# Kernel tuning notes

Hardware: AMD Instinct MI355X
Metric: run time of the kernel (lower is better)

Reference implementation:

```python
import jax, jax.numpy as jnp
import numpy as np

N, E, D = 50000, 800000, 128  # nodes, edges, in_dim=out_dim
LN_EPS = 1e-5


def setup_inputs() -> dict:
    key = jax.random.key(0)
    ks = jax.random.split(key, 8)
    x = jax.random.normal(ks[0], (N, D), dtype=jnp.float32)
    edge_index = jax.random.randint(ks[1], (2, E), 0, N, dtype=jnp.int64)
    edge_attr = jax.random.normal(ks[2], (E, D), dtype=jnp.float32)
    # message_net: Linear(2D -> D); update_net: Linear(2D -> D) + LayerNorm(D)
    s_msg = 1.0 / np.sqrt(2 * D)
    s_upd = 1.0 / np.sqrt(2 * D)
    W_msg = jax.random.uniform(ks[3], (2 * D, D), jnp.float32, -s_msg, s_msg)
    b_msg = jax.random.uniform(ks[4], (D,), jnp.float32, -s_msg, s_msg)
    W_upd = jax.random.uniform(ks[5], (2 * D, D), jnp.float32, -s_upd, s_upd)
    b_upd = jax.random.uniform(ks[6], (D,), jnp.float32, -s_upd, s_upd)
    gamma = jnp.ones((D,), jnp.float32)
    beta = jnp.zeros((D,), jnp.float32)
    return {"x": x, "edge_index": edge_index, "edge_attr": edge_attr,
            "W_msg": W_msg, "b_msg": b_msg, "W_upd": W_upd, "b_upd": b_upd,
            "gamma": gamma, "beta": beta}


def reference(x, edge_index, edge_attr, W_msg, b_msg, W_upd, b_upd, gamma, beta):
    src, dst = edge_index[0], edge_index[1]
    n = x.shape[0]
    # per-edge message: relu(Linear(concat[x_src, edge_attr]))  -> [E, D]
    msg_in = jnp.concatenate([x[src], edge_attr], axis=-1)
    msg = jax.nn.relu(msg_in @ W_msg + b_msg)
    # masked scatter-mean over destination nodes (zeros for isolated nodes)
    summed = jax.ops.segment_sum(msg, dst, num_segments=n)  # [N, D]
    counts = jax.ops.segment_sum(jnp.ones((msg.shape[0],), x.dtype), dst, num_segments=n)
    mean_msg = summed / jnp.maximum(counts, 1.0)[:, None]
    # update: Linear(concat[x, mean_msg]) + LayerNorm, residual (in_dim==out_dim), relu
    h = jnp.concatenate([x, mean_msg], axis=-1) @ W_upd + b_upd
    mu = jnp.mean(h, axis=-1, keepdims=True)
    var = jnp.mean(jnp.square(h - mu), axis=-1, keepdims=True)
    h = (h - mu) * jax.lax.rsqrt(var + LN_EPS) * gamma + beta
    return jax.nn.relu(h + x)
```

## Files before the change

kernel.cpp:

```cpp
#include <hip/hip_runtime.h>

#define LN_EPS 1e-5f

typedef __bf16 bf16x8 __attribute__((ext_vector_type(8)));
typedef unsigned short ushort8v __attribute__((ext_vector_type(8)));
typedef float f32x4 __attribute__((ext_vector_type(4)));

__device__ __forceinline__ float bf16_to_f(unsigned short u) {
    unsigned int x = ((unsigned int)u) << 16;
    return __builtin_bit_cast(float, x);
}
__device__ __forceinline__ unsigned short f_to_bf16(float f) {
    unsigned int u = __builtin_bit_cast(unsigned int, f);
    u += 0x7FFFu + ((u >> 16) & 1u);
    return (unsigned short)(u >> 16);
}
__device__ __forceinline__ int idx_at(const int* base, int i, int is64) {
    return is64 ? base[(long long)i << 1] : base[i];
}

template<int BF16>
__device__ __forceinline__ bf16x8 load_frag(const void* base, size_t off) {
    if (BF16) {
        return *(const bf16x8*)((const unsigned short*)base + off);
    } else {
        const float* p = (const float*)base + off;
        f32x4 a = *(const f32x4*)p;
        f32x4 b = *(const f32x4*)(p + 4);
        ushort8v u;
        u[0] = f_to_bf16(a[0]); u[1] = f_to_bf16(a[1]);
        u[2] = f_to_bf16(a[2]); u[3] = f_to_bf16(a[3]);
        u[4] = f_to_bf16(b[0]); u[5] = f_to_bf16(b[1]);
        u[6] = f_to_bf16(b[2]); u[7] = f_to_bf16(b[3]);
        return __builtin_bit_cast(bf16x8, u);
    }
}
template<int BF16>
__device__ __forceinline__ float load_sc(const void* base, size_t i) {
    return BF16 ? bf16_to_f(((const unsigned short*)base)[i]) : ((const float*)base)[i];
}
template<int BF16>
__device__ __forceinline__ void store_out(void* out, size_t i, float v) {
    if (BF16) ((unsigned short*)out)[i] = f_to_bf16(v);
    else      ((float*)out)[i] = v;
}

__global__ void detect_kernel(const unsigned short* __restrict__ xu,
                              const unsigned int* __restrict__ ei,
                              int N, int* __restrict__ flags)
{
    if (threadIdx.x != 0 || blockIdx.x != 0) return;
    int inrange = 0;
    for (int i = 0; i < 64; ++i) {
        unsigned short u = xu[2 * i];
        int e = (u >> 7) & 0xFF;
        if (e >= 0x60 && e <= 0x8A) inrange++;
    }
    int isbf16 = (inrange >= 48) ? 1 : 0;

    int is64 = 1;
    for (int i = 0; i < 64; ++i) {
        unsigned int lo = ei[2 * i], hi = ei[2 * i + 1];
        if (hi != 0u || lo >= (unsigned int)N) { is64 = 0; break; }
    }
    flags[0] = is64;
    flags[1] = isbf16;
}

__global__ __launch_bounds__(256) void zero_kernel(float* __restrict__ p, int n4)
{
    int i = blockIdx.x * 256 + threadIdx.x;
    if (i < n4) {
        f32x4 z = {0.f, 0.f, 0.f, 0.f};
        ((f32x4*)p)[i] = z;
    }
}

__global__ __launch_bounds__(256) void hist_kernel(
    const int* __restrict__ eidx, int* __restrict__ ecnt,
    const int* __restrict__ flags, int E)
{
    int e = blockIdx.x * 256 + threadIdx.x;
    if (e >= E) return;
    const int is64 = flags[0];
    const int* dstp = eidx + (is64 ? 2 * E : E);
    atomicAdd(&ecnt[idx_at(dstp, e, is64)], 1);
}

__global__ __launch_bounds__(1024) void scan_kernel(
    const int* __restrict__ ecnt, int* __restrict__ cursor, int N)
{
    __shared__ int sums[1024];
    const int t = threadIdx.x;
    const int chunk = (N + 1023) >> 10;
    const int s0 = t * chunk;
    const int s1 = (s0 + chunk < N) ? s0 + chunk : N;
    int sum = 0;
    for (int i = s0; i < s1; ++i) sum += ecnt[i];
    sums[t] = sum;
    __syncthreads();
    for (int ofs = 1; ofs < 1024; ofs <<= 1) {
        int v = sums[t];
        int add = (t >= ofs) ? sums[t - ofs] : 0;
        __syncthreads();
        sums[t] = v + add;
        __syncthreads();
    }
    int run = (t == 0) ? 0 : sums[t - 1];
    for (int i = s0; i < s1; ++i) { cursor[i] = run; run += ecnt[i]; }
}

__global__ __launch_bounds__(256) void scatter_kernel(
    const int* __restrict__ eidx, int* __restrict__ cursor,
    int* __restrict__ sorted_e, const int* __restrict__ flags, int E)
{
    int e = blockIdx.x * 256 + threadIdx.x;
    if (e >= E) return;
    const int is64 = flags[0];
    const int* dstp = eidx + (is64 ? 2 * E : E);
    int d = idx_at(dstp, e, is64);
    int pos = atomicAdd(&cursor[d], 1);
    sorted_e[pos] = e;
}

template<int BF16>
__global__ __launch_bounds__(256) void prep_transpose(
    const void* __restrict__ Wm, const void* __restrict__ Wu,
    unsigned short* __restrict__ WmT, unsigned short* __restrict__ WuT,
    const int* __restrict__ flags)
{
    if (flags[1] != BF16) return;
    int idx = blockIdx.x * 256 + threadIdx.x;
    int k = idx >> 7;
    int n = idx & 127;
    unsigned short wm, wu;
    if (BF16) {
        wm = ((const unsigned short*)Wm)[idx];
        wu = ((const unsigned short*)Wu)[idx];
    } else {
        wm = f_to_bf16(((const float*)Wm)[idx]);
        wu = f_to_bf16(((const float*)Wu)[idx]);
    }
    WmT[n * 256 + k] = wm;
    WuT[n * 256 + k] = wu;
}

template<int BF16>
__global__ __launch_bounds__(256) void edge_kernel(
    const void* __restrict__ x, const int* __restrict__ eidx,
    const void* __restrict__ ea, const unsigned short* __restrict__ WmT,
    const void* __restrict__ b_msg,
    float* __restrict__ sumbuf, const int* __restrict__ sorted_e,
    const int* __restrict__ flags, int E)
{
    if (flags[1] != BF16) return;
    const int is64 = flags[0];
    const int* srcp = eidx;
    const int* dstp = eidx + (is64 ? 2 * E : E);

    __shared__ int   eS[128];
    __shared__ int   dS[128];
    __shared__ float strip[2][16][132];

    const int pbase = blockIdx.x * 128;
    const int tid  = threadIdx.x;
    const int w    = tid >> 6;
    const int l    = tid & 63;
    const int m    = l & 15;
    const int quad = l >> 4;
    int valid = E - pbase; if (valid > 128) valid = 128;

    if (tid < 128) {
        int p = pbase + tid;
        int pc = p < E ? p : E - 1;
        int e = sorted_e[pc];
        eS[tid] = e;
        dS[tid] = idx_at(dstp, e, is64);
    }

    bf16x8 bfrag[2][8];
#pragma unroll
    for (int nt = 0; nt < 2; ++nt) {
        const unsigned short* p = WmT + (w * 32 + nt * 16 + m) * 256 + quad * 8;
#pragma unroll
        for (int kk = 0; kk < 8; ++kk)
            bfrag[nt][kk] = *(const bf16x8*)(p + kk * 32);
    }
    const float bias0 = load_sc<BF16>(b_msg, w * 32 + m);
    const float bias1 = load_sc<BF16>(b_msg, w * 32 + 16 + m);

    __syncthreads();

    int   cur_d   = -1;
    float cur_sum = 0.f;
    int   first   = 1;

    for (int mt = 0; mt < 8; ++mt) {
        const int b = mt & 1;
        const int e_a = eS[mt * 16 + m];
        const int sa  = idx_at(srcp, e_a, is64);
        const size_t xoff = (size_t)sa  * 128 + quad * 8;
        const size_t eoff = (size_t)e_a * 128 + quad * 8;

        f32x4 acc0 = {0.f, 0.f, 0.f, 0.f};
        f32x4 acc1 = {0.f, 0.f, 0.f, 0.f};
#pragma unroll
        for (int kk = 0; kk < 4; ++kk) {
            bf16x8 af = load_frag<BF16>(x, xoff + kk * 32);
            acc0 = __builtin_amdgcn_mfma_f32_16x16x32_bf16(af, bfrag[0][kk], acc0, 0, 0, 0);
            acc1 = __builtin_amdgcn_mfma_f32_16x16x32_bf16(af, bfrag[1][kk], acc1, 0, 0, 0);
        }
#pragma unroll
        for (int kk = 0; kk < 4; ++kk) {
            bf16x8 af = load_frag<BF16>(ea, eoff + kk * 32);
            acc0 = __builtin_amdgcn_mfma_f32_16x16x32_bf16(af, bfrag[0][kk + 4], acc0, 0, 0, 0);
            acc1 = __builtin_amdgcn_mfma_f32_16x16x32_bf16(af, bfrag[1][kk + 4], acc1, 0, 0, 0);
        }

#pragma unroll
        for (int i = 0; i < 4; ++i) {
            float v0 = acc0[i] + bias0; v0 = v0 > 0.f ? v0 : 0.f;
            float v1 = acc1[i] + bias1; v1 = v1 > 0.f ? v1 : 0.f;
            strip[b][quad * 4 + i][w * 32 + m]      = v0;
            strip[b][quad * 4 + i][w * 32 + 16 + m] = v1;
        }
        __syncthreads();

        if (tid < 128) {
            int rmax = valid - mt * 16; if (rmax > 16) rmax = 16;
            for (int r = 0; r < rmax; ++r) {
                int   d = dS[mt * 16 + r];
                float v = strip[b][r][tid];
                if (d == cur_d) {
                    cur_sum += v;
                } else {
                    if (cur_d >= 0) {
                        float* p = &sumbuf[(size_t)cur_d * 128 + tid];
                        if (first) { atomicAdd(p, cur_sum); first = 0; }
                        else       { *p = cur_sum; }
                    }
                    cur_d = d; cur_sum = v;
                }
            }
        }
    }
    if (tid < 128 && cur_d >= 0)
        atomicAdd(&sumbuf[(size_t)cur_d * 128 + tid], cur_sum);
}

template<int BF16>
__global__ __launch_bounds__(256) void node_kernel(
    const void* __restrict__ x,
    const float* __restrict__ sumbuf, const int* __restrict__ counts,
    const unsigned short* __restrict__ WuT, const void* __restrict__ b_upd,
    const void* __restrict__ gamma_, const void* __restrict__ beta_,
    void* __restrict__ out, const int* __restrict__ flags, int N)
{
    if (flags[1] != BF16) return;

    __shared__ float redS[4][64];
    __shared__ float redQ[4][64];
    __shared__ float muS[64];
    __shared__ float rsS[64];

    const int rbase = blockIdx.x * 64;
    const int tid  = threadIdx.x;
    const int w    = tid >> 6;
    const int l    = tid & 63;
    const int m    = l & 15;
    const int quad = l >> 4;

    bf16x8 bfrag[2][8];
#pragma unroll
    for (int nt = 0; nt < 2; ++nt) {
        const unsigned short* p = WuT + (w * 32 + nt * 16 + m) * 256 + quad * 8;
#pragma unroll
        for (int kk = 0; kk < 8; ++kk)
            bfrag[nt][kk] = *(const bf16x8*)(p + kk * 32);
    }
    const float bias0 = load_sc<BF16>(b_upd, w * 32 + m);
    const float bias1 = load_sc<BF16>(b_upd, w * 32 + 16 + m);

    f32x4 acc[4][2];

    for (int mt = 0; mt < 4; ++mt) {
        int r = rbase + mt * 16 + m;
        int rc = r < N ? r : N - 1;
        const size_t xoff = (size_t)rc * 128 + quad * 8;
        const float* srow = sumbuf + (size_t)rc * 128 + quad * 8;
        const float rcp = 1.0f / fmaxf((float)counts[rc], 1.0f);

        f32x4 a0 = {0.f, 0.f, 0.f, 0.f};
        f32x4 a1 = {0.f, 0.f, 0.f, 0.f};
#pragma unroll
        for (int kk = 0; kk < 4; ++kk) {
            bf16x8 af = load_frag<BF16>(x, xoff + kk * 32);
            a0 = __builtin_amdgcn_mfma_f32_16x16x32_bf16(af, bfrag[0][kk], a0, 0, 0, 0);
            a1 = __builtin_amdgcn_mfma_f32_16x16x32_bf16(af, bfrag[1][kk], a1, 0, 0, 0);
        }
#pragma unroll
        for (int kk = 0; kk < 4; ++kk) {
            const float* sp = srow + kk * 32;
            ushort8v uu;
#pragma unroll
            for (int j = 0; j < 8; ++j) uu[j] = f_to_bf16(sp[j] * rcp);
            bf16x8 av = __builtin_bit_cast(bf16x8, uu);
            a0 = __builtin_amdgcn_mfma_f32_16x16x32_bf16(av, bfrag[0][kk + 4], a0, 0, 0, 0);
            a1 = __builtin_amdgcn_mfma_f32_16x16x32_bf16(av, bfrag[1][kk + 4], a1, 0, 0, 0);
        }

        float ps[4], qs[4];
#pragma unroll
        for (int i = 0; i < 4; ++i) {
            a0[i] += bias0;
            a1[i] += bias1;
            ps[i] = a0[i] + a1[i];
            qs[i] = a0[i] * a0[i] + a1[i] * a1[i];
        }
        acc[mt][0] = a0;
        acc[mt][1] = a1;

#pragma unroll
        for (int s = 1; s < 16; s <<= 1) {
#pragma unroll
            for (int i = 0; i < 4; ++i) {
                ps[i] += __shfl_xor(ps[i], s, 64);
                qs[i] += __shfl_xor(qs[i], s, 64);
            }
        }
        if (m == 0) {
#pragma unroll
            for (int i = 0; i < 4; ++i) {
                redS[w][mt * 16 + quad * 4 + i] = ps[i];
                redQ[w][mt * 16 + quad * 4 + i] = qs[i];
            }
        }
    }
    __syncthreads();

    if (tid < 64) {
        float s = redS[0][tid] + redS[1][tid] + redS[2][tid] + redS[3][tid];
        float q = redQ[0][tid] + redQ[1][tid] + redQ[2][tid] + redQ[3][tid];
        float mu = s * (1.0f / 128.0f);
        float var = q * (1.0f / 128.0f) - mu * mu;
        muS[tid] = mu;
        rsS[tid] = rsqrtf(var + LN_EPS);
    }
    __syncthreads();

    const float g0  = load_sc<BF16>(gamma_, w * 32 + m);
    const float be0 = load_sc<BF16>(beta_,  w * 32 + m);
    const float g1  = load_sc<BF16>(gamma_, w * 32 + 16 + m);
    const float be1 = load_sc<BF16>(beta_,  w * 32 + 16 + m);

    for (int mt = 0; mt < 4; ++mt) {
#pragma unroll
        for (int i = 0; i < 4; ++i) {
            const int ridx = mt * 16 + quad * 4 + i;
            const int r = rbase + ridx;
            if (r < N) {
                const float mu = muS[ridx];
                const float rs = rsS[ridx];
                const size_t c0 = (size_t)r * 128 + w * 32 + m;
                const size_t c1 = c0 + 16;
                float v0 = (acc[mt][0][i] - mu) * rs * g0 + be0 + load_sc<BF16>(x, c0);
                float v1 = (acc[mt][1][i] - mu) * rs * g1 + be1 + load_sc<BF16>(x, c1);
                store_out<BF16>(out, c0, v0 > 0.f ? v0 : 0.f);
                store_out<BF16>(out, c1, v1 > 0.f ? v1 : 0.f);
            }
        }
    }
}

extern "C" void kernel_launch(void* const* d_in, const int* in_sizes, int n_in,
                              void* d_out, int out_size, void* d_ws, size_t ws_size,
                              hipStream_t stream)
{
    const void* x  = d_in[0];
    const int*  ei = (const int*)d_in[1];
    const void* ea = d_in[2];
    const void* Wm = d_in[3];
    const void* bm = d_in[4];
    const void* Wu = d_in[5];
    const void* bu = d_in[6];
    const void* gm = d_in[7];
    const void* bt = d_in[8];

    const int N = in_sizes[0] / 128;
    const int E = in_sizes[2] / 128;

    char* ws = (char*)d_ws;
    int*   flags    = (int*)ws;
    float* sumbuf   = (float*)(ws + 16);
    int*   ecnt     = (int*)(ws + 16 + (size_t)N * 512);
    int*   cursor   = ecnt + N;
    int*   sorted_e = cursor + N;
    unsigned short* WmT = (unsigned short*)(sorted_e + E);
    unsigned short* WuT = WmT + 256 * 128;

    detect_kernel<<<1, 64, 0, stream>>>((const unsigned short*)x,
                                        (const unsigned int*)ei, N, flags);

    const int n4 = (N * 129 + 3) / 4;
    zero_kernel<<<(n4 + 255) / 256, 256, 0, stream>>>(sumbuf, n4);

    const int eb256 = (E + 255) / 256;
    hist_kernel<<<eb256, 256, 0, stream>>>(ei, ecnt, flags, E);
    scan_kernel<<<1, 1024, 0, stream>>>(ecnt, cursor, N);
    scatter_kernel<<<eb256, 256, 0, stream>>>(ei, cursor, sorted_e, flags, E);

    prep_transpose<0><<<128, 256, 0, stream>>>(Wm, Wu, WmT, WuT, flags);
    prep_transpose<1><<<128, 256, 0, stream>>>(Wm, Wu, WmT, WuT, flags);

    const int eblocks = (E + 127) / 128;
    edge_kernel<0><<<eblocks, 256, 0, stream>>>(x, ei, ea, WmT, bm, sumbuf, sorted_e, flags, E);
    edge_kernel<1><<<eblocks, 256, 0, stream>>>(x, ei, ea, WmT, bm, sumbuf, sorted_e, flags, E);

    const int nblocks = (N + 63) / 64;
    node_kernel<0><<<nblocks, 256, 0, stream>>>(x, sumbuf, ecnt, WuT, bu, gm, bt, d_out, flags, N);
    node_kernel<1><<<nblocks, 256, 0, stream>>>(x, sumbuf, ecnt, WuT, bu, gm, bt, d_out, flags, N);
}
```

Baseline: 1.134 ms.

## Parallelize scan, pre-sort src/dst indices, pre-convert x to bf16, restructure edge reduction

Replaces the single-block serial scan with a three-kernel multi-block scan. The scatter step now writes sorted src and dst arrays alongside the edge id, so the edge kernel no longer chases indices. x is converted to bf16 once, which halves the gather traffic in the edge and node kernels. The edge kernel computes all 128 messages into one shared buffer with a single barrier, then reduces in two halves, replacing the per-tile syncs. The costs are extra workspace, extra launches and more shared memory per block, which can lower occupancy.

```diff
diff --git a/kernel.cpp b/kernel.cpp
--- a/kernel.cpp
+++ b/kernel.cpp
@@ -49,22 +49,18 @@
                               const unsigned int* __restrict__ ei,
                               int N, int* __restrict__ flags)
 {
-    if (threadIdx.x != 0 || blockIdx.x != 0) return;
-    int inrange = 0;
-    for (int i = 0; i < 64; ++i) {
-        unsigned short u = xu[2 * i];
-        int e = (u >> 7) & 0xFF;
-        if (e >= 0x60 && e <= 0x8A) inrange++;
-    }
-    int isbf16 = (inrange >= 48) ? 1 : 0;
-
-    int is64 = 1;
-    for (int i = 0; i < 64; ++i) {
-        unsigned int lo = ei[2 * i], hi = ei[2 * i + 1];
-        if (hi != 0u || lo >= (unsigned int)N) { is64 = 0; break; }
-    }
-    flags[0] = is64;
-    flags[1] = isbf16;
+    const int t = threadIdx.x;
+    unsigned short u = xu[2 * t];
+    int e = (u >> 7) & 0xFF;
+    int okb = (e >= 0x60 && e <= 0x8A) ? 1 : 0;
+    unsigned long long bb = __ballot(okb);
+    unsigned int lo = ei[2 * t], hi = ei[2 * t + 1];
+    int ok64 = (hi == 0u && lo < (unsigned int)N) ? 1 : 0;
+    unsigned long long b64 = __ballot(ok64);
+    if (t == 0) {
+        flags[1] = (__popcll(bb) >= 48) ? 1 : 0;
+        flags[0] = (b64 == ~0ull) ? 1 : 0;
+    }
 }
 
 __global__ __launch_bounds__(256) void zero_kernel(float* __restrict__ p, int n4)
@@ -87,40 +83,109 @@
     atomicAdd(&ecnt[idx_at(dstp, e, is64)], 1);
 }
 
-__global__ __launch_bounds__(1024) void scan_kernel(
-    const int* __restrict__ ecnt, int* __restrict__ cursor, int N)
-{
-    __shared__ int sums[1024];
+__global__ __launch_bounds__(256) void scan_partial(
+    const int* __restrict__ ecnt, int* __restrict__ bsum, int N)
+{
+    __shared__ int red[256];
     const int t = threadIdx.x;
-    const int chunk = (N + 1023) >> 10;
-    const int s0 = t * chunk;
-    const int s1 = (s0 + chunk < N) ? s0 + chunk : N;
-    int sum = 0;
-    for (int i = s0; i < s1; ++i) sum += ecnt[i];
-    sums[t] = sum;
+    const int base = blockIdx.x * 1024 + t * 4;
+    int s = 0;
+    if (base + 3 < N) {
+        int4 v = *(const int4*)(ecnt + base);
+        s = v.x + v.y + v.z + v.w;
+    } else {
+        for (int j = 0; j < 4; ++j) if (base + j < N) s += ecnt[base + j];
+    }
+    red[t] = s;
     __syncthreads();
-    for (int ofs = 1; ofs < 1024; ofs <<= 1) {
-        int v = sums[t];
-        int add = (t >= ofs) ? sums[t - ofs] : 0;
+    for (int ofs = 128; ofs > 0; ofs >>= 1) {
+        if (t < ofs) red[t] += red[t + ofs];
         __syncthreads();
-        sums[t] = v + add;
+    }
+    if (t == 0) bsum[blockIdx.x] = red[0];
+}
+
+__global__ void scan_base(const int* __restrict__ bsum,
+                          int* __restrict__ bbase, int nb)
+{
+    if (threadIdx.x != 0) return;
+    int run = 0;
+    for (int i = 0; i < nb; ++i) { bbase[i] = run; run += bsum[i]; }
+}
+
+__global__ __launch_bounds__(256) void scan_final(
+    const int* __restrict__ ecnt, const int* __restrict__ bbase,
+    int* __restrict__ cursor, int N)
+{
+    __shared__ int tsum[256];
+    const int t = threadIdx.x;
+    const int base = blockIdx.x * 1024 + t * 4;
+    int v0 = 0, v1 = 0, v2 = 0, v3 = 0;
+    if (base + 3 < N) {
+        int4 u = *(const int4*)(ecnt + base);
+        v0 = u.x; v1 = u.y; v2 = u.z; v3 = u.w;
+    } else {
+        if (base + 0 < N) v0 = ecnt[base + 0];
+        if (base + 1 < N) v1 = ecnt[base + 1];
+        if (base + 2 < N) v2 = ecnt[base + 2];
+        if (base + 3 < N) v3 = ecnt[base + 3];
+    }
+    tsum[t] = v0 + v1 + v2 + v3;
+    __syncthreads();
+    for (int ofs = 1; ofs < 256; ofs <<= 1) {
+        int val = tsum[t];
+        int add = (t >= ofs) ? tsum[t - ofs] : 0;
         __syncthreads();
-    }
-    int run = (t == 0) ? 0 : sums[t - 1];
-    for (int i = s0; i < s1; ++i) { cursor[i] = run; run += ecnt[i]; }
+        tsum[t] = val + add;
+        __syncthreads();
+    }
+    int excl = (t == 0 ? 0 : tsum[t - 1]) + bbase[blockIdx.x];
+    int c0 = excl, c1 = c0 + v0, c2 = c1 + v1, c3 = c2 + v2;
+    if (base + 3 < N) {
+        int4 o = {c0, c1, c2, c3};
+        *(int4*)(cursor + base) = o;
+    } else {
+        if (base + 0 < N) cursor[base + 0] = c0;
+        if (base + 1 < N) cursor[base + 1] = c1;
+        if (base + 2 < N) cursor[base + 2] = c2;
+        if (base + 3 < N) cursor[base + 3] = c3;
+    }
 }
 
 __global__ __launch_bounds__(256) void scatter_kernel(
     const int* __restrict__ eidx, int* __restrict__ cursor,
-    int* __restrict__ sorted_e, const int* __restrict__ flags, int E)
+    int* __restrict__ se, int* __restrict__ ss, int* __restrict__ sd,
+    const int* __restrict__ flags, int E)
 {
     int e = blockIdx.x * 256 + threadIdx.x;
     if (e >= E) return;
     const int is64 = flags[0];
+    const int* srcp = eidx;
     const int* dstp = eidx + (is64 ? 2 * E : E);
     int d = idx_at(dstp, e, is64);
+    int s = idx_at(srcp, e, is64);
     int pos = atomicAdd(&cursor[d], 1);
-    sorted_e[pos] = e;
+    se[pos] = e;
+    ss[pos] = s;
+    sd[pos] = d;
+}
+
+__global__ __launch_bounds__(256) void convert_x(
+    const float* __restrict__ x, unsigned short* __restrict__ xb,
+    int n8, const int* __restrict__ flags)
+{
+    if (flags[1]) return;
+    int i = blockIdx.x * 256 + threadIdx.x;
+    if (i >= n8) return;
+    const float* p = x + (size_t)i * 8;
+    f32x4 a = *(const f32x4*)p;
+    f32x4 b = *(const f32x4*)(p + 4);
+    ushort8v u;
+    u[0] = f_to_bf16(a[0]); u[1] = f_to_bf16(a[1]);
+    u[2] = f_to_bf16(a[2]); u[3] = f_to_bf16(a[3]);
+    u[4] = f_to_bf16(b[0]); u[5] = f_to_bf16(b[1]);
+    u[6] = f_to_bf16(b[2]); u[7] = f_to_bf16(b[3]);
+    *(ushort8v*)(xb + (size_t)i * 8) = u;
 }
 
 template<int BF16>
@@ -147,20 +212,18 @@
 
 template<int BF16>
 __global__ __launch_bounds__(256) void edge_kernel(
-    const void* __restrict__ x, const int* __restrict__ eidx,
+    const unsigned short* __restrict__ xb,
     const void* __restrict__ ea, const unsigned short* __restrict__ WmT,
     const void* __restrict__ b_msg,
-    float* __restrict__ sumbuf, const int* __restrict__ sorted_e,
+    float* __restrict__ sumbuf,
+    const int* __restrict__ se, const int* __restrict__ ss,
+    const int* __restrict__ sd,
     const int* __restrict__ flags, int E)
 {
     if (flags[1] != BF16) return;
-    const int is64 = flags[0];
-    const int* srcp = eidx;
-    const int* dstp = eidx + (is64 ? 2 * E : E);
-
-    __shared__ int   eS[128];
-    __shared__ int   dS[128];
-    __shared__ float strip[2][16][132];
+
+    __shared__ float msgbuf[128][130];
+    __shared__ int dS[128];
 
     const int pbase = blockIdx.x * 128;
     const int tid  = threadIdx.x;
@@ -172,10 +235,16 @@
 
     if (tid < 128) {
         int p = pbase + tid;
-        int pc = p < E ? p : E - 1;
-        int e = sorted_e[pc];
-        eS[tid] = e;
-        dS[tid] = idx_at(dstp, e, is64);
+        dS[tid] = sd[p < E ? p : E - 1];
+    }
+
+    int my_e[8], my_s[8];
+#pragma unroll
+    for (int mt = 0; mt < 8; ++mt) {
+        int p = pbase + mt * 16 + m;
+        if (p >= E) p = E - 1;
+        my_e[mt] = se[p];
+        my_s[mt] = ss[p];
     }
 
     bf16x8 bfrag[2][8];
@@ -189,24 +258,16 @@
     const float bias0 = load_sc<BF16>(b_msg, w * 32 + m);
     const float bias1 = load_sc<BF16>(b_msg, w * 32 + 16 + m);
 
-    __syncthreads();
-
-    int   cur_d   = -1;
-    float cur_sum = 0.f;
-    int   first   = 1;
-
+#pragma unroll
     for (int mt = 0; mt < 8; ++mt) {
-        const int b = mt & 1;
-        const int e_a = eS[mt * 16 + m];
-        const int sa  = idx_at(srcp, e_a, is64);
-        const size_t xoff = (size_t)sa  * 128 + quad * 8;
-        const size_t eoff = (size_t)e_a * 128 + quad * 8;
+        const size_t xoff = (size_t)my_s[mt] * 128 + quad * 8;
+        const size_t eoff = (size_t)my_e[mt] * 128 + quad * 8;
 
         f32x4 acc0 = {0.f, 0.f, 0.f, 0.f};
         f32x4 acc1 = {0.f, 0.f, 0.f, 0.f};
 #pragma unroll
         for (int kk = 0; kk < 4; ++kk) {
-            bf16x8 af = load_frag<BF16>(x, xoff + kk * 32);
+            bf16x8 af = *(const bf16x8*)(xb + xoff + kk * 32);
             acc0 = __builtin_amdgcn_mfma_f32_16x16x32_bf16(af, bfrag[0][kk], acc0, 0, 0, 0);
             acc1 = __builtin_amdgcn_mfma_f32_16x16x32_bf16(af, bfrag[1][kk], acc1, 0, 0, 0);
         }
@@ -221,36 +282,40 @@
         for (int i = 0; i < 4; ++i) {
             float v0 = acc0[i] + bias0; v0 = v0 > 0.f ? v0 : 0.f;
             float v1 = acc1[i] + bias1; v1 = v1 > 0.f ? v1 : 0.f;
-            strip[b][quad * 4 + i][w * 32 + m]      = v0;
-            strip[b][quad * 4 + i][w * 32 + 16 + m] = v1;
-        }
-        __syncthreads();
-
-        if (tid < 128) {
-            int rmax = valid - mt * 16; if (rmax > 16) rmax = 16;
-            for (int r = 0; r < rmax; ++r) {
-                int   d = dS[mt * 16 + r];
-                float v = strip[b][r][tid];
-                if (d == cur_d) {
-                    cur_sum += v;
-                } else {
-                    if (cur_d >= 0) {
-                        float* p = &sumbuf[(size_t)cur_d * 128 + tid];
-                        if (first) { atomicAdd(p, cur_sum); first = 0; }
-                        else       { *p = cur_sum; }
-                    }
-                    cur_d = d; cur_sum = v;
-                }
+            const int row = mt * 16 + quad * 4 + i;
+            msgbuf[row][w * 32 + m]      = v0;
+            msgbuf[row][w * 32 + 16 + m] = v1;
+        }
+    }
+    __syncthreads();
+
+    const int half = tid >> 7;
+    const int col  = tid & 127;
+    const int r0 = half * 64;
+    int r1 = r0 + 64; if (r1 > valid) r1 = valid;
+    if (r0 < r1) {
+        int   cur_d = dS[r0];
+        float s     = msgbuf[r0][col];
+        int   first = 1;
+        for (int r = r0 + 1; r < r1; ++r) {
+            float v = msgbuf[r][col];
+            int   d = dS[r];
+            if (d == cur_d) {
+                s += v;
+            } else {
+                float* p = &sumbuf[(size_t)cur_d * 128 + col];
+                if (first) { atomicAdd(p, s); first = 0; }
+                else       { *p = s; }
+                cur_d = d; s = v;
             }
         }
-    }
-    if (tid < 128 && cur_d >= 0)
-        atomicAdd(&sumbuf[(size_t)cur_d * 128 + tid], cur_sum);
+        atomicAdd(&sumbuf[(size_t)cur_d * 128 + col], s);
+    }
 }
 
 template<int BF16>
 __global__ __launch_bounds__(256) void node_kernel(
-    const void* __restrict__ x,
+    const void* __restrict__ x, const unsigned short* __restrict__ xbn,
     const float* __restrict__ sumbuf, const int* __restrict__ counts,
     const unsigned short* __restrict__ WuT, const void* __restrict__ b_upd,
     const void* __restrict__ gamma_, const void* __restrict__ beta_,
@@ -294,7 +359,7 @@
         f32x4 a1 = {0.f, 0.f, 0.f, 0.f};
 #pragma unroll
         for (int kk = 0; kk < 4; ++kk) {
-            bf16x8 af = load_frag<BF16>(x, xoff + kk * 32);
+            bf16x8 af = *(const bf16x8*)(xbn + xoff + kk * 32);
             a0 = __builtin_amdgcn_mfma_f32_16x16x32_bf16(af, bfrag[0][kk], a0, 0, 0, 0);
             a1 = __builtin_amdgcn_mfma_f32_16x16x32_bf16(af, bfrag[1][kk], a1, 0, 0, 0);
         }
@@ -394,8 +459,13 @@
     float* sumbuf   = (float*)(ws + 16);
     int*   ecnt     = (int*)(ws + 16 + (size_t)N * 512);
     int*   cursor   = ecnt + N;
-    int*   sorted_e = cursor + N;
-    unsigned short* WmT = (unsigned short*)(sorted_e + E);
+    int*   bsum     = cursor + N;
+    int*   bbase    = bsum + 256;
+    int*   se       = bbase + 256;
+    int*   ss       = se + E;
+    int*   sd       = ss + E;
+    unsigned short* xb  = (unsigned short*)(sd + E);
+    unsigned short* WmT = xb + (size_t)N * 128;
     unsigned short* WuT = WmT + 256 * 128;
 
     detect_kernel<<<1, 64, 0, stream>>>((const unsigned short*)x,
@@ -406,17 +476,27 @@
 
     const int eb256 = (E + 255) / 256;
     hist_kernel<<<eb256, 256, 0, stream>>>(ei, ecnt, flags, E);
-    scan_kernel<<<1, 1024, 0, stream>>>(ecnt, cursor, N);
-    scatter_kernel<<<eb256, 256, 0, stream>>>(ei, cursor, sorted_e, flags, E);
+
+    const int nb = (N + 1023) / 1024;
+    scan_partial<<<nb, 256, 0, stream>>>(ecnt, bsum, N);
+    scan_base<<<1, 64, 0, stream>>>(bsum, bbase, nb);
+    scan_final<<<nb, 256, 0, stream>>>(ecnt, bbase, cursor, N);
+
+    scatter_kernel<<<eb256, 256, 0, stream>>>(ei, cursor, se, ss, sd, flags, E);
+
+    const int n8 = N * 16;
+    convert_x<<<(n8 + 255) / 256, 256, 0, stream>>>((const float*)x, xb, n8, flags);
 
     prep_transpose<0><<<128, 256, 0, stream>>>(Wm, Wu, WmT, WuT, flags);
     prep_transpose<1><<<128, 256, 0, stream>>>(Wm, Wu, WmT, WuT, flags);
 
     const int eblocks = (E + 127) / 128;
-    edge_kernel<0><<<eblocks, 256, 0, stream>>>(x, ei, ea, WmT, bm, sumbuf, sorted_e, flags, E);
-    edge_kernel<1><<<eblocks, 256, 0, stream>>>(x, ei, ea, WmT, bm, sumbuf, sorted_e, flags, E);
+    edge_kernel<0><<<eblocks, 256, 0, stream>>>(xb, ea, WmT, bm, sumbuf, se, ss, sd, flags, E);
+    edge_kernel<1><<<eblocks, 256, 0, stream>>>((const unsigned short*)x, ea, WmT, bm,
+                                                sumbuf, se, ss, sd, flags, E);
 
     const int nblocks = (N + 63) / 64;
-    node_kernel<0><<<nblocks, 256, 0, stream>>>(x, sumbuf, ecnt, WuT, bu, gm, bt, d_out, flags, N);
-    node_kernel<1><<<nblocks, 256, 0, stream>>>(x, sumbuf, ecnt, WuT, bu, gm, bt, d_out, flags, N);
-}
+    node_kernel<0><<<nblocks, 256, 0, stream>>>(x, xb, sumbuf, ecnt, WuT, bu, gm, bt, d_out, flags, N);
+    node_kernel<1><<<nblocks, 256, 0, stream>>>(x, (const unsigned short*)x, sumbuf, ecnt,
+                                                WuT, bu, gm, bt, d_out, flags, N);
+}
```

Measured after the change: 943.5 us. 1.2x faster.
